# Kernel optimization log

Measured on AMD Instinct MI355X. Metric: run time of the kernel, lower is better.

The kernel has to match this reference:

```python
import jax, jax.numpy as jnp
import numpy as np

N = 16  # lpcoeffs_N, LPC order


def setup_inputs() -> dict:
    key = jax.random.key(0)
    # [B, T, N] LPC coefficients; small magnitude keeps (1 - ki^2) well-conditioned
    x = (jax.random.uniform(key, (64, 32768, N), dtype=jnp.float32) - 0.5) * 0.2
    return {"x": x}


def reference(x):
    # Levinson step-down: LPC -> reflection coefficients (RC).
    # At step i, split into leading j-1 coeffs `a` and already-finalized tail `b`.
    # ki is the current reflection coefficient (first element of the tail).
    for i in range(1, N):
        j = N - i + 1
        a = x[:, :, : j - 1]          # [B, T, j-1]
        b = x[:, :, j - 1 :]          # [B, T, N-j+1]
        ki = b[:, :, 0:1]             # [B, T, 1], broadcasts over last axis
        temp = (a - ki * a[:, :, ::-1]) / (1.0 - ki * ki)
        x = jnp.concatenate([temp, b], axis=2)  # [B, T, N]
    return x
```

## Files before the change

### kernel.cpp

```cpp
#include <hip/hip_runtime.h>


constexpr int N = 16;

__global__ __launch_bounds__(256) void lpc2rc_kernel(const float* __restrict__ x,
                                                     float* __restrict__ out,
                                                     int nrows) {
    const int r = blockIdx.x * blockDim.x + threadIdx.x;
    if (r >= nrows) return;

    const float4* __restrict__ in4 = (const float4*)x;
    float4* __restrict__ out4 = (float4*)out;

    float4 v0 = in4[r * 4 + 0];
    float4 v1 = in4[r * 4 + 1];
    float4 v2 = in4[r * 4 + 2];
    float4 v3 = in4[r * 4 + 3];

    float a[N];
    a[0]  = v0.x; a[1]  = v0.y; a[2]  = v0.z; a[3]  = v0.w;
    a[4]  = v1.x; a[5]  = v1.y; a[6]  = v1.z; a[7]  = v1.w;
    a[8]  = v2.x; a[9]  = v2.y; a[10] = v2.z; a[11] = v2.w;
    a[12] = v3.x; a[13] = v3.y; a[14] = v3.z; a[15] = v3.w;

#pragma unroll
    for (int i = 1; i < N; ++i) {
        const int len = N - i;
        const float k = a[len];
        const float inv = __builtin_amdgcn_rcpf(1.0f - k * k);
#pragma unroll
        for (int m = 0; m < len / 2; ++m) {
            const int j = len - 1 - m;
            const float am = a[m];
            const float aj = a[j];
            a[m] = (am - k * aj) * inv;
            a[j] = (aj - k * am) * inv;
        }
        if (len & 1) {
            const int mid = len / 2;
            const float amid = a[mid];
            a[mid] = (amid - k * amid) * inv;
        }
    }

    v0.x = a[0];  v0.y = a[1];  v0.z = a[2];  v0.w = a[3];
    v1.x = a[4];  v1.y = a[5];  v1.z = a[6];  v1.w = a[7];
    v2.x = a[8];  v2.y = a[9];  v2.z = a[10]; v2.w = a[11];
    v3.x = a[12]; v3.y = a[13]; v3.z = a[14]; v3.w = a[15];

    out4[r * 4 + 0] = v0;
    out4[r * 4 + 1] = v1;
    out4[r * 4 + 2] = v2;
    out4[r * 4 + 3] = v3;
}

extern "C" void kernel_launch(void* const* d_in, const int* in_sizes, int n_in,
                              void* d_out, int out_size, void* d_ws, size_t ws_size,
                              hipStream_t stream) {
    const float* x = (const float*)d_in[0];
    float* out = (float*)d_out;
    const int nrows = in_sizes[0] / N;

    const int block = 256;
    const int grid = (nrows + block - 1) / block;
    lpc2rc_kernel<<<grid, block, 0, stream>>>(x, out, nrows);
}
```

Baseline: 233.8 us.

## Stage rows through padded LDS for fully coalesced float4 loads and stores

Each wave now loads its 64 rows with lane-contiguous float4 accesses, so consecutive lanes read consecutive 16-byte chunks. It then transposes the data through a padded LDS tile (stride 17) so each lane can work on its own row in registers, and transposes back through LDS before the coalesced store. The aim is to remove the strided per-thread 64-byte accesses of the old layout, at the cost of extra LDS traffic and shared memory per workgroup. A fallback path keeps the original per-thread access pattern for partial waves at the tail.

```diff
diff --git a/kernel.cpp b/kernel.cpp
--- a/kernel.cpp
+++ b/kernel.cpp
@@ -2,56 +2,114 @@
 
 
 constexpr int N = 16;
+constexpr int RS = 17;
+constexpr int WAVES_PER_WG = 4;
 
 __global__ __launch_bounds__(256) void lpc2rc_kernel(const float* __restrict__ x,
                                                      float* __restrict__ out,
                                                      int nrows) {
-    const int r = blockIdx.x * blockDim.x + threadIdx.x;
-    if (r >= nrows) return;
+    __shared__ float lds[WAVES_PER_WG * 64 * RS];
 
-    const float4* __restrict__ in4 = (const float4*)x;
-    float4* __restrict__ out4 = (float4*)out;
+    const int tid  = threadIdx.x;
+    const int wave = tid >> 6;
+    const int lane = tid & 63;
+    float* __restrict__ wlds = lds + wave * 64 * RS;
 
-    float4 v0 = in4[r * 4 + 0];
-    float4 v1 = in4[r * 4 + 1];
-    float4 v2 = in4[r * 4 + 2];
-    float4 v3 = in4[r * 4 + 3];
+    const long long wave_row0 = ((long long)blockIdx.x * WAVES_PER_WG + wave) * 64;
 
     float a[N];
-    a[0]  = v0.x; a[1]  = v0.y; a[2]  = v0.z; a[3]  = v0.w;
-    a[4]  = v1.x; a[5]  = v1.y; a[6]  = v1.z; a[7]  = v1.w;
-    a[8]  = v2.x; a[9]  = v2.y; a[10] = v2.z; a[11] = v2.w;
-    a[12] = v3.x; a[13] = v3.y; a[14] = v3.z; a[15] = v3.w;
+
+    if (wave_row0 + 64 <= (long long)nrows) {
+        const float4* __restrict__ in4 = (const float4*)x;
+        float4* __restrict__ out4 = (float4*)out;
+        const long long base4 = wave_row0 * 4;
+
+        float4 ld[4];
+#pragma unroll
+        for (int c = 0; c < 4; ++c)
+            ld[c] = in4[base4 + (long long)(c * 64 + lane)];
 
 #pragma unroll
-    for (int i = 1; i < N; ++i) {
-        const int len = N - i;
-        const float k = a[len];
-        const float inv = __builtin_amdgcn_rcpf(1.0f - k * k);
+        for (int c = 0; c < 4; ++c) {
+            float* p = wlds + (16 * c + (lane >> 2)) * RS + 4 * (lane & 3);
+            p[0] = ld[c].x; p[1] = ld[c].y; p[2] = ld[c].z; p[3] = ld[c].w;
+        }
+
+        {
+            const float* p = wlds + lane * RS;
 #pragma unroll
-        for (int m = 0; m < len / 2; ++m) {
-            const int j = len - 1 - m;
-            const float am = a[m];
-            const float aj = a[j];
-            a[m] = (am - k * aj) * inv;
-            a[j] = (aj - k * am) * inv;
+            for (int e = 0; e < N; ++e) a[e] = p[e];
         }
-        if (len & 1) {
-            const int mid = len / 2;
-            const float amid = a[mid];
-            a[mid] = (amid - k * amid) * inv;
+
+#pragma unroll
+        for (int i = 1; i < N; ++i) {
+            const int len = N - i;
+            const float k = a[len];
+            const float inv = __builtin_amdgcn_rcpf(1.0f - k * k);
+#pragma unroll
+            for (int m = 0; m < len / 2; ++m) {
+                const int j = len - 1 - m;
+                const float am = a[m];
+                const float aj = a[j];
+                a[m] = (am - k * aj) * inv;
+                a[j] = (aj - k * am) * inv;
+            }
+            if (len & 1) {
+                const int mid = len / 2;
+                const float amid = a[mid];
+                a[mid] = (amid - k * amid) * inv;
+            }
         }
+
+        {
+            float* p = wlds + lane * RS;
+#pragma unroll
+            for (int e = 0; e < N; ++e) p[e] = a[e];
+        }
+
+#pragma unroll
+        for (int c = 0; c < 4; ++c) {
+            const float* p = wlds + (16 * c + (lane >> 2)) * RS + 4 * (lane & 3);
+            float4 v;
+            v.x = p[0]; v.y = p[1]; v.z = p[2]; v.w = p[3];
+            out4[base4 + (long long)(c * 64 + lane)] = v;
+        }
+    } else {
+        const long long r = wave_row0 + lane;
+        if (r >= (long long)nrows) return;
+        const float4* __restrict__ in4 = (const float4*)x;
+        float4* __restrict__ out4 = (float4*)out;
+        float4 v0 = in4[r * 4 + 0], v1 = in4[r * 4 + 1],
+               v2 = in4[r * 4 + 2], v3 = in4[r * 4 + 3];
+        a[0]=v0.x; a[1]=v0.y; a[2]=v0.z; a[3]=v0.w;
+        a[4]=v1.x; a[5]=v1.y; a[6]=v1.z; a[7]=v1.w;
+        a[8]=v2.x; a[9]=v2.y; a[10]=v2.z; a[11]=v2.w;
+        a[12]=v3.x; a[13]=v3.y; a[14]=v3.z; a[15]=v3.w;
+#pragma unroll
+        for (int i = 1; i < N; ++i) {
+            const int len = N - i;
+            const float k = a[len];
+            const float inv = __builtin_amdgcn_rcpf(1.0f - k * k);
+#pragma unroll
+            for (int m = 0; m < len / 2; ++m) {
+                const int j = len - 1 - m;
+                const float am = a[m], aj = a[j];
+                a[m] = (am - k * aj) * inv;
+                a[j] = (aj - k * am) * inv;
+            }
+            if (len & 1) {
+                const int mid = len / 2;
+                const float amid = a[mid];
+                a[mid] = (amid - k * amid) * inv;
+            }
+        }
+        v0.x=a[0]; v0.y=a[1]; v0.z=a[2]; v0.w=a[3];
+        v1.x=a[4]; v1.y=a[5]; v1.z=a[6]; v1.w=a[7];
+        v2.x=a[8]; v2.y=a[9]; v2.z=a[10]; v2.w=a[11];
+        v3.x=a[12]; v3.y=a[13]; v3.z=a[14]; v3.w=a[15];
+        out4[r * 4 + 0] = v0; out4[r * 4 + 1] = v1;
+        out4[r * 4 + 2] = v2; out4[r * 4 + 3] = v3;
     }
-
-    v0.x = a[0];  v0.y = a[1];  v0.z = a[2];  v0.w = a[3];
-    v1.x = a[4];  v1.y = a[5];  v1.z = a[6];  v1.w = a[7];
-    v2.x = a[8];  v2.y = a[9];  v2.z = a[10]; v2.w = a[11];
-    v3.x = a[12]; v3.y = a[13]; v3.z = a[14]; v3.w = a[15];
-
-    out4[r * 4 + 0] = v0;
-    out4[r * 4 + 1] = v1;
-    out4[r * 4 + 2] = v2;
-    out4[r * 4 + 3] = v3;
 }
 
 extern "C" void kernel_launch(void* const* d_in, const int* in_sizes, int n_in,
@@ -60,8 +118,7 @@
     const float* x = (const float*)d_in[0];
     float* out = (float*)d_out;
     const int nrows = in_sizes[0] / N;
-
-    const int block = 256;
-    const int grid = (nrows + block - 1) / block;
-    lpc2rc_kernel<<<grid, block, 0, stream>>>(x, out, nrows);
+    const int rows_per_wg = 64 * WAVES_PER_WG;
+    const int grid = (nrows + rows_per_wg - 1) / rows_per_wg;
+    lpc2rc_kernel<<<grid, 256, 0, stream>>>(x, out, nrows);
 }
```

Measured after the change: 229.7 us. Within noise of the previous version (-1.7%).
